# Performance work log

Hardware: AMD Instinct MI355X
Metric: run time of the kernel (lower is better)

Reference implementation:

```python
import jax, jax.numpy as jnp
import numpy as np


def setup_inputs() -> dict:
    key = jax.random.key(0)
    ks = jax.random.split(key, 4)
    B, H, W, C = 4, 64, 64, 256
    Ck = C // 8
    x = jax.random.normal(ks[0], (B, H, W, C), dtype=jnp.float32)
    Wf = jax.random.normal(ks[1], (C, Ck), dtype=jnp.float32) * (1.0 / np.sqrt(C))
    Wg = jax.random.normal(ks[2], (C, Ck), dtype=jnp.float32) * (1.0 / np.sqrt(C))
    Wh = jax.random.normal(ks[3], (C, C), dtype=jnp.float32) * (1.0 / np.sqrt(C))
    bf = jnp.zeros((Ck,), jnp.float32)
    bg = jnp.zeros((Ck,), jnp.float32)
    bh = jnp.zeros((C,), jnp.float32)
    gamma = jnp.ones((1,), jnp.float32)
    return {"x": x, "Wf": Wf, "bf": bf, "Wg": Wg, "bg": bg, "Wh": Wh, "bh": bh, "gamma": gamma}


def reference(x, Wf, bf, Wg, bg, Wh, bh, gamma):
    B, H, W, C = x.shape
    N = H * W
    xf = x.reshape(B, N, C)  # hw_flatten; 1x1 conv == per-pixel matmul
    f = xf @ Wf + bf          # [B, N, C//8] (keys)
    g = xf @ Wg + bg          # [B, N, C//8] (queries)
    h = xf @ Wh + bh          # [B, N, C]    (values)
    s = jnp.einsum('bnk,bmk->bnm', g, f)   # [B, N, N], no scaling (as in source)
    b = jax.nn.softmax(s, axis=-1)
    o = jnp.einsum('bnm,bmc->bnc', b, h)   # [B, N, C]
    y = gamma * o.reshape(B, H, W, C) + x
    return y
```

## Files before the change

### kernel.cpp

```cpp
#include <hip/hip_runtime.h>
#include <stdint.h>

typedef short short8 __attribute__((ext_vector_type(8)));
typedef short short4_t __attribute__((ext_vector_type(4)));
typedef float f32x4 __attribute__((ext_vector_type(4)));

__device__ __forceinline__ float bf2f(unsigned short u) {
    union { unsigned int i; float f; } v; v.i = ((unsigned int)u) << 16; return v.f;
}
__device__ __forceinline__ unsigned short f2bf(float f) {
    union { float f; unsigned int i; } v; v.f = f;
    return (unsigned short)((v.i + 0x8000u) >> 16);
}

__global__ __launch_bounds__(256) void k_pre(const float* __restrict__ x,
                                             const float* __restrict__ Wf,
                                             const float* __restrict__ Wg,
                                             const float* __restrict__ Wh,
                                             unsigned short* __restrict__ xh,
                                             unsigned short* __restrict__ xl,
                                             unsigned short* __restrict__ wTh,
                                             unsigned short* __restrict__ wTl) {
    if (blockIdx.x < 2048) {
        int gid = blockIdx.x * 256 + threadIdx.x;
        const float* src = x + (size_t)gid * 8;
        f32x4 a0 = *(const f32x4*)src;
        f32x4 a1 = *(const f32x4*)(src + 4);
        short8 sh, sl;
#pragma unroll
        for (int j = 0; j < 4; ++j) {
            unsigned short h0 = f2bf(a0[j]);
            sh[j] = (short)h0; sl[j] = (short)f2bf(a0[j] - bf2f(h0));
            unsigned short h1 = f2bf(a1[j]);
            sh[4 + j] = (short)h1; sl[4 + j] = (short)f2bf(a1[j] - bf2f(h1));
        }
        *(short8*)&xh[(size_t)gid * 8] = sh;
        *(short8*)&xl[(size_t)gid * 8] = sl;
    } else {
        int col = blockIdx.x - 2048;
        int k = threadIdx.x;
        float v;
        if (col < 32) v = Wf[k * 32 + col];
        else if (col < 64) v = Wg[k * 32 + (col - 32)];
        else v = Wh[k * 256 + (col - 64)];
        unsigned short h = f2bf(v);
        wTh[col * 256 + k] = h;
        if (col < 64) wTl[col * 256 + k] = f2bf(v - bf2f(h));
    }
}

__global__ __launch_bounds__(256) void k_proj(
    const unsigned short* __restrict__ xh,
    const unsigned short* __restrict__ xl,
    const unsigned short* __restrict__ wTh,
    const unsigned short* __restrict__ wTl,
    const float* __restrict__ bfb,
    const float* __restrict__ bgb,
    const float* __restrict__ bhb,
    unsigned short* __restrict__ fKh,
    unsigned short* __restrict__ fKl,
    unsigned short* __restrict__ gQh,
    unsigned short* __restrict__ gQl,
    unsigned short* __restrict__ hT) {
    __shared__ short sm[4 * 64 * 72];
    int tid = threadIdx.x;
    int wave = tid >> 6, lane = tid & 63, lq = lane & 15, quad = lane >> 4;
    int rt = blockIdx.x;
    const unsigned short* xhb = xh + (size_t)rt * 64 * 256;
    const unsigned short* xlb = xl + (size_t)rt * 64 * 256;
    f32x4 zero4 = {0.f, 0.f, 0.f, 0.f};

    if (blockIdx.y < 4) {
        const int XO = 0, WO = 64 * 136;
        int cb = blockIdx.y;
        const unsigned short* wbase = wTh + (size_t)(64 + cb * 64) * 256;
        f32x4 acc[4] = {zero4, zero4, zero4, zero4};

        for (int ph = 0; ph < 2; ++ph) {
            int k0 = ph * 128;
            __syncthreads();
#pragma unroll
            for (int u = 0; u < 4; ++u) {
                int q = u * 256 + tid;
                int row = q >> 4, kc = q & 15;
                *(short8*)&sm[XO + row * 136 + kc * 8] =
                    *(const short8*)&xhb[row * 256 + k0 + kc * 8];
                *(short8*)&sm[WO + row * 136 + kc * 8] =
                    *(const short8*)&wbase[row * 256 + k0 + kc * 8];
            }
            __syncthreads();
#pragma unroll
            for (int ks = 0; ks < 4; ++ks) {
                short8 a = *(const short8*)&sm[XO + (wave * 16 + lq) * 136 + ks * 32 + quad * 8];
#pragma unroll
                for (int ct = 0; ct < 4; ++ct) {
                    short8 bfr = *(const short8*)&sm[WO + (lq + 16 * ct) * 136 + ks * 32 + quad * 8];
                    acc[ct] = __builtin_amdgcn_mfma_f32_16x16x32_bf16(a, bfr, acc[ct], 0, 0, 0);
                }
            }
        }

        int rowl = wave * 16 + quad * 4;
        int grow0 = rt * 64;
        int bidx = grow0 >> 12, n0 = (grow0 & 4095) + rowl;
#pragma unroll
        for (int ct = 0; ct < 4; ++ct) {
            int c = cb * 64 + lq + 16 * ct;
            float bias = bhb[c];
            short4_t pk;
#pragma unroll
            for (int r = 0; r < 4; ++r) pk[r] = (short)f2bf(acc[ct][r] + bias);
            size_t a8 = (((size_t)(bidx * 16 + (c >> 4)) * 128 + (n0 >> 5)) * 64 +
                         ((n0 & 31) >> 3) * 16 + (c & 15)) * 8 + (n0 & 7);
            *(short4_t*)&hT[a8] = pk;
        }
    } else {
        const int XH = 0, XL = 64 * 72, WH = 2 * 64 * 72, WL = 3 * 64 * 72;
        f32x4 acc[4] = {zero4, zero4, zero4, zero4};

        for (int ph = 0; ph < 4; ++ph) {
            int k0 = ph * 64;
            __syncthreads();
#pragma unroll
            for (int u = 0; u < 2; ++u) {
                int q = u * 256 + tid;
                int row = q >> 3, kc = q & 7;
                *(short8*)&sm[XH + row * 72 + kc * 8] =
                    *(const short8*)&xhb[row * 256 + k0 + kc * 8];
                *(short8*)&sm[XL + row * 72 + kc * 8] =
                    *(const short8*)&xlb[row * 256 + k0 + kc * 8];
                *(short8*)&sm[WH + row * 72 + kc * 8] =
                    *(const short8*)&wTh[row * 256 + k0 + kc * 8];
                *(short8*)&sm[WL + row * 72 + kc * 8] =
                    *(const short8*)&wTl[row * 256 + k0 + kc * 8];
            }
            __syncthreads();
#pragma unroll
            for (int ks = 0; ks < 2; ++ks) {
                short8 ah = *(const short8*)&sm[XH + (wave * 16 + lq) * 72 + ks * 32 + quad * 8];
                short8 al = *(const short8*)&sm[XL + (wave * 16 + lq) * 72 + ks * 32 + quad * 8];
#pragma unroll
                for (int ct = 0; ct < 4; ++ct) {
                    short8 bh = *(const short8*)&sm[WH + (lq + 16 * ct) * 72 + ks * 32 + quad * 8];
                    short8 bl = *(const short8*)&sm[WL + (lq + 16 * ct) * 72 + ks * 32 + quad * 8];
                    acc[ct] = __builtin_amdgcn_mfma_f32_16x16x32_bf16(ah, bh, acc[ct], 0, 0, 0);
                    acc[ct] = __builtin_amdgcn_mfma_f32_16x16x32_bf16(al, bh, acc[ct], 0, 0, 0);
                    acc[ct] = __builtin_amdgcn_mfma_f32_16x16x32_bf16(ah, bl, acc[ct], 0, 0, 0);
                }
            }
        }

        int rowl = wave * 16 + quad * 4;
#pragma unroll
        for (int ct = 0; ct < 4; ++ct) {
            int coll = lq + 16 * ct;
#pragma unroll
            for (int r = 0; r < 4; ++r) {
                int grow = rt * 64 + rowl + r;
                int bidx = grow >> 12, n = grow & 4095;
                float v = acc[ct][r];
                size_t o = (size_t)(bidx * 256 + (n >> 4)) * 512 +
                           (((coll & 31) >> 3) * 16 + (n & 15)) * 8 + (coll & 7);
                if (coll < 32) {
                    v += bfb[coll];
                    unsigned short h = f2bf(v);
                    fKh[o] = h;
                    fKl[o] = f2bf(v - bf2f(h));
                } else {
                    int cg = coll - 32;
                    size_t og = (size_t)(bidx * 256 + (n >> 4)) * 512 +
                                ((cg >> 3) * 16 + (n & 15)) * 8 + (cg & 7);
                    v += bgb[cg];
                    unsigned short h = f2bf(v);
                    gQh[og] = h;
                    gQl[og] = f2bf(v - bf2f(h));
                }
            }
        }
    }
}

#define PSTR 136
__global__ __launch_bounds__(512, 4) void k_attn(
    const unsigned short* __restrict__ fKh,
    const unsigned short* __restrict__ fKl,
    const unsigned short* __restrict__ gQh,
    const unsigned short* __restrict__ gQl,
    const unsigned short* __restrict__ hT,
    const float* __restrict__ x,
    const float* __restrict__ gam_p,
    float* __restrict__ out) {
    __shared__ short Ps[2][32 * PSTR];
    __shared__ float Lred[2][16][4];
    int tid = threadIdx.x;
    int wave = tid >> 6, lane = tid & 63, lq = lane & 15, quad = lane >> 4;
    int b = blockIdx.x & 3;
    int qt = blockIdx.x >> 2;
    int rs = wave >> 2;
    int kt4 = wave & 3;
    int lchunk = quad * 16 + lq;

    const unsigned short* fhB = fKh + (size_t)b * 131072;
    const unsigned short* flB = fKl + (size_t)b * 131072;
    const unsigned short* hB  = hT + (size_t)b * 1048576;

    f32x4 zero4 = {0.f, 0.f, 0.f, 0.f};
    f32x4 acc[4];
#pragma unroll
    for (int i = 0; i < 4; ++i) acc[i] = zero4;
    float l_part[4] = {0.f, 0.f, 0.f, 0.f};

    int gtile = b * 256 + qt * 2 + rs;
    short8 ghfrag = *(const short8*)&gQh[(size_t)gtile * 512 + lchunk * 8];
    short8 glfrag = *(const short8*)&gQl[(size_t)gtile * 512 + lchunk * 8];

    size_t fo0 = (size_t)kt4 * 512 + lchunk * 8;
    const unsigned short* hp = hB + (size_t)(wave * 2) * 65536;
    size_t ho0 = (size_t)lchunk * 8;

    short8 fh0 = *(const short8*)&fhB[fo0];
    short8 fh1 = *(const short8*)&fhB[fo0 + 2048];
    short8 fl0 = *(const short8*)&flB[fo0];
    short8 fl1 = *(const short8*)&flB[fo0 + 2048];
    short8 hb[2][4];
#pragma unroll
    for (int ct = 0; ct < 2; ++ct)
#pragma unroll
        for (int kk = 0; kk < 4; ++kk)
            hb[ct][kk] = *(const short8*)&hp[ho0 + ct * 65536 + kk * 512];

    for (int t = 0; t < 32; ++t) {
        int p = t & 1;
        __builtin_amdgcn_s_setprio(1);
        f32x4 S0 = __builtin_amdgcn_mfma_f32_16x16x32_bf16(ghfrag, fh0, zero4, 0, 0, 0);
        f32x4 S1 = __builtin_amdgcn_mfma_f32_16x16x32_bf16(ghfrag, fh1, zero4, 0, 0, 0);
        S0 = __builtin_amdgcn_mfma_f32_16x16x32_bf16(glfrag, fh0, S0, 0, 0, 0);
        S1 = __builtin_amdgcn_mfma_f32_16x16x32_bf16(glfrag, fh1, S1, 0, 0, 0);
        S0 = __builtin_amdgcn_mfma_f32_16x16x32_bf16(ghfrag, fl0, S0, 0, 0, 0);
        S1 = __builtin_amdgcn_mfma_f32_16x16x32_bf16(ghfrag, fl1, S1, 0, 0, 0);
        __builtin_amdgcn_s_setprio(0);

        {
            size_t fo = (size_t)(t < 31 ? t + 1 : t) * 4096 + fo0;
            fh0 = *(const short8*)&fhB[fo];
            fh1 = *(const short8*)&fhB[fo + 2048];
            fl0 = *(const short8*)&flB[fo];
            fl1 = *(const short8*)&flB[fo + 2048];
        }

#pragma unroll
        for (int r = 0; r < 4; ++r) {
            S0[r] = __expf(S0[r]);
            S1[r] = __expf(S1[r]);
            l_part[r] += S0[r] + S1[r];
        }
#pragma unroll
        for (int r = 0; r < 4; ++r) {
            int row = rs * 16 + quad * 4 + r;
            Ps[p][row * PSTR + kt4 * 16 + lq] = (short)f2bf(S0[r]);
            Ps[p][row * PSTR + 64 + kt4 * 16 + lq] = (short)f2bf(S1[r]);
        }

        __syncthreads();

        __builtin_amdgcn_s_setprio(1);
#pragma unroll
        for (int rb = 0; rb < 2; ++rb) {
            short8 pa[4];
#pragma unroll
            for (int kk = 0; kk < 4; ++kk)
                pa[kk] = *(const short8*)&Ps[p][(rb * 16 + lq) * PSTR + kk * 32 + quad * 8];
#pragma unroll
            for (int kk = 0; kk < 4; ++kk) {
                acc[rb * 2 + 0] = __builtin_amdgcn_mfma_f32_16x16x32_bf16(pa[kk], hb[0][kk], acc[rb * 2 + 0], 0, 0, 0);
                acc[rb * 2 + 1] = __builtin_amdgcn_mfma_f32_16x16x32_bf16(pa[kk], hb[1][kk], acc[rb * 2 + 1], 0, 0, 0);
            }
        }
        __builtin_amdgcn_s_setprio(0);

        {
            size_t ho = (size_t)(t < 31 ? t + 1 : t) * 2048 + ho0;
#pragma unroll
            for (int ct = 0; ct < 2; ++ct)
#pragma unroll
                for (int kk = 0; kk < 4; ++kk)
                    hb[ct][kk] = *(const short8*)&hp[ho + ct * 65536 + kk * 512];
        }
    }

#pragma unroll
    for (int r = 0; r < 4; ++r) {
        float s = l_part[r];
        s += __shfl_xor(s, 1);
        s += __shfl_xor(s, 2);
        s += __shfl_xor(s, 4);
        s += __shfl_xor(s, 8);
        if (lq == 0) Lred[rs][quad * 4 + r][kt4] = s;
    }
    __syncthreads();

    float gam = gam_p[0];
#pragma unroll
    for (int rb = 0; rb < 2; ++rb)
#pragma unroll
        for (int r = 0; r < 4; ++r) {
            float l = Lred[rb][quad * 4 + r][0] + Lred[rb][quad * 4 + r][1] +
                      Lred[rb][quad * 4 + r][2] + Lred[rb][quad * 4 + r][3];
            float linv = 1.0f / l;
            int n = qt * 32 + rb * 16 + quad * 4 + r;
            size_t rowo = ((size_t)(b * 4096 + n)) * 256;
#pragma unroll
            for (int ct = 0; ct < 2; ++ct) {
                int c = wave * 32 + ct * 16 + lq;
                out[rowo + c] = gam * (acc[rb * 2 + ct][r] * linv) + x[rowo + c];
            }
        }
}

extern "C" void kernel_launch(void* const* d_in, const int* in_sizes, int n_in,
                              void* d_out, int out_size, void* d_ws, size_t ws_size,
                              hipStream_t stream) {
    const float* x   = (const float*)d_in[0];
    const float* Wf  = (const float*)d_in[1];
    const float* bfb = (const float*)d_in[2];
    const float* Wg  = (const float*)d_in[3];
    const float* bgb = (const float*)d_in[4];
    const float* Wh  = (const float*)d_in[5];
    const float* bhb = (const float*)d_in[6];
    const float* gam = (const float*)d_in[7];
    float* out = (float*)d_out;

    char* ws = (char*)d_ws;
    const size_t MI = 1u << 20;
    unsigned short* xh  = (unsigned short*)(ws);
    unsigned short* xl  = (unsigned short*)(ws + 8 * MI);
    unsigned short* fKh = (unsigned short*)(ws + 16 * MI);
    unsigned short* fKl = (unsigned short*)(ws + 17 * MI);
    unsigned short* gQh = (unsigned short*)(ws + 18 * MI);
    unsigned short* gQl = (unsigned short*)(ws + 19 * MI);
    unsigned short* hT  = (unsigned short*)(ws + 20 * MI);
    unsigned short* wTh = (unsigned short*)(ws + 28 * MI);
    unsigned short* wTl = (unsigned short*)(ws + 28 * MI + 160 * 1024);

    k_pre<<<dim3(2368), dim3(256), 0, stream>>>(x, Wf, Wg, Wh, xh, xl, wTh, wTl);
    k_proj<<<dim3(256, 5), dim3(256), 0, stream>>>(xh, xl, wTh, wTl, bfb, bgb, bhb,
                                                   fKh, fKl, gQh, gQl, hT);
    k_attn<<<dim3(512), dim3(512), 0, stream>>>(fKh, fKl, gQh, gQl, hT,
                                                x, gam, out);
}
```

Baseline: 158.2 us.

## Enlarge attention tile to 64 query rows with LDS-shared key tiles

The attention kernel now runs 1024-thread blocks that each cover 64 query rows instead of 32, with half as many blocks. Each wave produces 64 output channels for one 16-row slice. Key tiles (hi and lo parts) are loaded cooperatively into a double-buffered LDS buffer and shared by all waves, instead of each wave reading them from global memory. The aim is to halve per-block global traffic for the value matrix and remove duplicated key loads. In exchange, value fragments are no longer prefetched a full iteration ahead; they are loaded inside the same iteration, which exposes more memory latency, and the larger block adds register and LDS pressure.

```diff
diff --git a/kernel.cpp b/kernel.cpp
--- a/kernel.cpp
+++ b/kernel.cpp
@@ -181,7 +181,7 @@
 }
 
 #define PSTR 136
-__global__ __launch_bounds__(512, 4) void k_attn(
+__global__ __launch_bounds__(1024, 4) void k_attn(
     const unsigned short* __restrict__ fKh,
     const unsigned short* __restrict__ fKl,
     const unsigned short* __restrict__ gQh,
@@ -190,14 +190,15 @@
     const float* __restrict__ x,
     const float* __restrict__ gam_p,
     float* __restrict__ out) {
-    __shared__ short Ps[2][32 * PSTR];
-    __shared__ float Lred[2][16][4];
+    __shared__ short Ps[2][64 * PSTR];
+    __shared__ short Fb[2][2][4096];
+    __shared__ float Lred[4][16][4];
     int tid = threadIdx.x;
     int wave = tid >> 6, lane = tid & 63, lq = lane & 15, quad = lane >> 4;
     int b = blockIdx.x & 3;
     int qt = blockIdx.x >> 2;
     int rs = wave >> 2;
-    int kt4 = wave & 3;
+    int kc = wave & 3;
     int lchunk = quad * 16 + lq;
 
     const unsigned short* fhB = fKh + (size_t)b * 131072;
@@ -210,27 +211,41 @@
     for (int i = 0; i < 4; ++i) acc[i] = zero4;
     float l_part[4] = {0.f, 0.f, 0.f, 0.f};
 
-    int gtile = b * 256 + qt * 2 + rs;
+    int gtile = b * 256 + qt * 4 + rs;
     short8 ghfrag = *(const short8*)&gQh[(size_t)gtile * 512 + lchunk * 8];
     short8 glfrag = *(const short8*)&gQl[(size_t)gtile * 512 + lchunk * 8];
 
-    size_t fo0 = (size_t)kt4 * 512 + lchunk * 8;
-    const unsigned short* hp = hB + (size_t)(wave * 2) * 65536;
+    int sid = tid & 511;
+    int hl = tid >> 9;
+    const unsigned short* fB0 = hl ? flB : fhB;
+
+    const unsigned short* hp = hB + (size_t)(kc * 4) * 65536;
     size_t ho0 = (size_t)lchunk * 8;
 
-    short8 fh0 = *(const short8*)&fhB[fo0];
-    short8 fh1 = *(const short8*)&fhB[fo0 + 2048];
-    short8 fl0 = *(const short8*)&flB[fo0];
-    short8 fl1 = *(const short8*)&flB[fo0 + 2048];
-    short8 hb[2][4];
-#pragma unroll
-    for (int ct = 0; ct < 2; ++ct)
-#pragma unroll
-        for (int kk = 0; kk < 4; ++kk)
-            hb[ct][kk] = *(const short8*)&hp[ho0 + ct * 65536 + kk * 512];
+    size_t foS0 = (size_t)(kc * 2) * 512 + lchunk * 8;
+
+    *(short8*)&Fb[0][hl][sid * 8] = *(const short8*)&fB0[sid * 8];
+    __syncthreads();
 
     for (int t = 0; t < 32; ++t) {
         int p = t & 1;
+        size_t tbase = (size_t)t * 2048;
+
+        int nt = (t < 31) ? t + 1 : t;
+        short8 fn = *(const short8*)&fB0[(size_t)nt * 4096 + sid * 8];
+        short8 hb00 = *(const short8*)&hp[ho0 + 0 * 65536 + tbase];
+        short8 hb10 = *(const short8*)&hp[ho0 + 1 * 65536 + tbase];
+        short8 hb20 = *(const short8*)&hp[ho0 + 2 * 65536 + tbase];
+        short8 hb30 = *(const short8*)&hp[ho0 + 3 * 65536 + tbase];
+        short8 hb01 = *(const short8*)&hp[ho0 + 0 * 65536 + tbase + 512];
+        short8 hb11 = *(const short8*)&hp[ho0 + 1 * 65536 + tbase + 512];
+        short8 hb21 = *(const short8*)&hp[ho0 + 2 * 65536 + tbase + 512];
+        short8 hb31 = *(const short8*)&hp[ho0 + 3 * 65536 + tbase + 512];
+
+        short8 fh0 = *(const short8*)&Fb[p][0][foS0];
+        short8 fl0 = *(const short8*)&Fb[p][1][foS0];
+        short8 fh1 = *(const short8*)&Fb[p][0][foS0 + 512];
+        short8 fl1 = *(const short8*)&Fb[p][1][foS0 + 512];
         __builtin_amdgcn_s_setprio(1);
         f32x4 S0 = __builtin_amdgcn_mfma_f32_16x16x32_bf16(ghfrag, fh0, zero4, 0, 0, 0);
         f32x4 S1 = __builtin_amdgcn_mfma_f32_16x16x32_bf16(ghfrag, fh1, zero4, 0, 0, 0);
@@ -240,14 +255,6 @@
         S1 = __builtin_amdgcn_mfma_f32_16x16x32_bf16(ghfrag, fl1, S1, 0, 0, 0);
         __builtin_amdgcn_s_setprio(0);
 
-        {
-            size_t fo = (size_t)(t < 31 ? t + 1 : t) * 4096 + fo0;
-            fh0 = *(const short8*)&fhB[fo];
-            fh1 = *(const short8*)&fhB[fo + 2048];
-            fl0 = *(const short8*)&flB[fo];
-            fl1 = *(const short8*)&flB[fo + 2048];
-        }
-
 #pragma unroll
         for (int r = 0; r < 4; ++r) {
             S0[r] = __expf(S0[r]);
@@ -257,35 +264,47 @@
 #pragma unroll
         for (int r = 0; r < 4; ++r) {
             int row = rs * 16 + quad * 4 + r;
-            Ps[p][row * PSTR + kt4 * 16 + lq] = (short)f2bf(S0[r]);
-            Ps[p][row * PSTR + 64 + kt4 * 16 + lq] = (short)f2bf(S1[r]);
-        }
+            Ps[p][row * PSTR + kc * 32 + lq] = (short)f2bf(S0[r]);
+            Ps[p][row * PSTR + kc * 32 + 16 + lq] = (short)f2bf(S1[r]);
+        }
+
+        *(short8*)&Fb[1 - p][hl][sid * 8] = fn;
 
         __syncthreads();
 
+        short8 hc02 = *(const short8*)&hp[ho0 + 0 * 65536 + tbase + 1024];
+        short8 hc12 = *(const short8*)&hp[ho0 + 1 * 65536 + tbase + 1024];
+        short8 hc22 = *(const short8*)&hp[ho0 + 2 * 65536 + tbase + 1024];
+        short8 hc32 = *(const short8*)&hp[ho0 + 3 * 65536 + tbase + 1024];
+        short8 hc03 = *(const short8*)&hp[ho0 + 0 * 65536 + tbase + 1536];
+        short8 hc13 = *(const short8*)&hp[ho0 + 1 * 65536 + tbase + 1536];
+        short8 hc23 = *(const short8*)&hp[ho0 + 2 * 65536 + tbase + 1536];
+        short8 hc33 = *(const short8*)&hp[ho0 + 3 * 65536 + tbase + 1536];
+
+        int prow = (rs * 16 + lq) * PSTR + quad * 8;
+        short8 pa0 = *(const short8*)&Ps[p][prow];
+        short8 pa1 = *(const short8*)&Ps[p][prow + 32];
+        short8 pa2 = *(const short8*)&Ps[p][prow + 64];
+        short8 pa3 = *(const short8*)&Ps[p][prow + 96];
+
         __builtin_amdgcn_s_setprio(1);
-#pragma unroll
-        for (int rb = 0; rb < 2; ++rb) {
-            short8 pa[4];
-#pragma unroll
-            for (int kk = 0; kk < 4; ++kk)
-                pa[kk] = *(const short8*)&Ps[p][(rb * 16 + lq) * PSTR + kk * 32 + quad * 8];
-#pragma unroll
-            for (int kk = 0; kk < 4; ++kk) {
-                acc[rb * 2 + 0] = __builtin_amdgcn_mfma_f32_16x16x32_bf16(pa[kk], hb[0][kk], acc[rb * 2 + 0], 0, 0, 0);
-                acc[rb * 2 + 1] = __builtin_amdgcn_mfma_f32_16x16x32_bf16(pa[kk], hb[1][kk], acc[rb * 2 + 1], 0, 0, 0);
-            }
-        }
+        acc[0] = __builtin_amdgcn_mfma_f32_16x16x32_bf16(pa0, hb00, acc[0], 0, 0, 0);
+        acc[1] = __builtin_amdgcn_mfma_f32_16x16x32_bf16(pa0, hb10, acc[1], 0, 0, 0);
+        acc[2] = __builtin_amdgcn_mfma_f32_16x16x32_bf16(pa0, hb20, acc[2], 0, 0, 0);
+        acc[3] = __builtin_amdgcn_mfma_f32_16x16x32_bf16(pa0, hb30, acc[3], 0, 0, 0);
+        acc[0] = __builtin_amdgcn_mfma_f32_16x16x32_bf16(pa1, hb01, acc[0], 0, 0, 0);
+        acc[1] = __builtin_amdgcn_mfma_f32_16x16x32_bf16(pa1, hb11, acc[1], 0, 0, 0);
+        acc[2] = __builtin_amdgcn_mfma_f32_16x16x32_bf16(pa1, hb21, acc[2], 0, 0, 0);
+        acc[3] = __builtin_amdgcn_mfma_f32_16x16x32_bf16(pa1, hb31, acc[3], 0, 0, 0);
+        acc[0] = __builtin_amdgcn_mfma_f32_16x16x32_bf16(pa2, hc02, acc[0], 0, 0, 0);
+        acc[1] = __builtin_amdgcn_mfma_f32_16x16x32_bf16(pa2, hc12, acc[1], 0, 0, 0);
+        acc[2] = __builtin_amdgcn_mfma_f32_16x16x32_bf16(pa2, hc22, acc[2], 0, 0, 0);
+        acc[3] = __builtin_amdgcn_mfma_f32_16x16x32_bf16(pa2, hc32, acc[3], 0, 0, 0);
+        acc[0] = __builtin_amdgcn_mfma_f32_16x16x32_bf16(pa3, hc03, acc[0], 0, 0, 0);
+        acc[1] = __builtin_amdgcn_mfma_f32_16x16x32_bf16(pa3, hc13, acc[1], 0, 0, 0);
+        acc[2] = __builtin_amdgcn_mfma_f32_16x16x32_bf16(pa3, hc23, acc[2], 0, 0, 0);
+        acc[3] = __builtin_amdgcn_mfma_f32_16x16x32_bf16(pa3, hc33, acc[3], 0, 0, 0);
         __builtin_amdgcn_s_setprio(0);
-
-        {
-            size_t ho = (size_t)(t < 31 ? t + 1 : t) * 2048 + ho0;
-#pragma unroll
-            for (int ct = 0; ct < 2; ++ct)
-#pragma unroll
-                for (int kk = 0; kk < 4; ++kk)
-                    hb[ct][kk] = *(const short8*)&hp[ho + ct * 65536 + kk * 512];
-        }
     }
 
 #pragma unroll
@@ -295,26 +314,24 @@
         s += __shfl_xor(s, 2);
         s += __shfl_xor(s, 4);
         s += __shfl_xor(s, 8);
-        if (lq == 0) Lred[rs][quad * 4 + r][kt4] = s;
+        if (lq == 0) Lred[rs][quad * 4 + r][kc] = s;
     }
     __syncthreads();
 
     float gam = gam_p[0];
 #pragma unroll
-    for (int rb = 0; rb < 2; ++rb)
-#pragma unroll
-        for (int r = 0; r < 4; ++r) {
-            float l = Lred[rb][quad * 4 + r][0] + Lred[rb][quad * 4 + r][1] +
-                      Lred[rb][quad * 4 + r][2] + Lred[rb][quad * 4 + r][3];
-            float linv = 1.0f / l;
-            int n = qt * 32 + rb * 16 + quad * 4 + r;
-            size_t rowo = ((size_t)(b * 4096 + n)) * 256;
-#pragma unroll
-            for (int ct = 0; ct < 2; ++ct) {
-                int c = wave * 32 + ct * 16 + lq;
-                out[rowo + c] = gam * (acc[rb * 2 + ct][r] * linv) + x[rowo + c];
-            }
-        }
+    for (int r = 0; r < 4; ++r) {
+        float l = Lred[rs][quad * 4 + r][0] + Lred[rs][quad * 4 + r][1] +
+                  Lred[rs][quad * 4 + r][2] + Lred[rs][quad * 4 + r][3];
+        float linv = 1.0f / l;
+        int n = qt * 64 + rs * 16 + quad * 4 + r;
+        size_t rowo = ((size_t)(b * 4096 + n)) * 256;
+#pragma unroll
+        for (int ct = 0; ct < 4; ++ct) {
+            int c = kc * 64 + ct * 16 + lq;
+            out[rowo + c] = gam * (acc[ct][r] * linv) + x[rowo + c];
+        }
+    }
 }
 
 extern "C" void kernel_launch(void* const* d_in, const int* in_sizes, int n_in,
@@ -345,6 +362,6 @@
     k_pre<<<dim3(2368), dim3(256), 0, stream>>>(x, Wf, Wg, Wh, xh, xl, wTh, wTl);
     k_proj<<<dim3(256, 5), dim3(256), 0, stream>>>(xh, xl, wTh, wTl, bfb, bgb, bhb,
                                                    fKh, fKl, gQh, gQl, hT);
-    k_attn<<<dim3(512), dim3(512), 0, stream>>>(fKh, fKl, gQh, gQl, hT,
-                                                x, gam, out);
-}
+    k_attn<<<dim3(256), dim3(1024), 0, stream>>>(fKh, fKl, gQh, gQl, hT,
+                                                 x, gam, out);
+}
```

Measured after the change: 171.1 us. 8.2% more time.
